# Optimization experiments

Hardware: AMD Instinct MI355X
Metric: run time of the kernel (lower is better)

Reference implementation:

```python
import jax, jax.numpy as jnp
import numpy as np


def setup_inputs() -> dict:
    key = jax.random.key(0)
    k1, k2, k3, k4 = jax.random.split(key, 4)
    B, T, C, H = 8, 2048, 1024, 128
    x = jax.random.normal(k1, (B, T, C), dtype=jnp.float32)
    Wq = jax.random.normal(k2, (C, H), dtype=jnp.float32) * (C ** -0.5)
    Wk = jax.random.normal(k3, (C, H), dtype=jnp.float32) * (C ** -0.5)
    Wv = jax.random.normal(k4, (C, H), dtype=jnp.float32) * (C ** -0.5)
    return {
        "x": x, "Wq": Wq, "Wk": Wk, "Wv": Wv,
        "gamma_fast_logit": jnp.float32(0.0),
        "gamma_medium_logit": jnp.float32(2.0),
        "gamma_slow_logit": jnp.float32(4.0),
        "alpha_logits": jnp.zeros((3,), dtype=jnp.float32),
    }


def _temporal_bias(T, gamma_fast_logit, gamma_medium_logit, gamma_slow_logit, alpha_logits):
    # delta_t[i,j] = max(i-j, 0)
    i = jnp.arange(T)[:, None]
    j = jnp.arange(T)[None, :]
    delta_t = jnp.maximum(i - j, 0).astype(jnp.float32)  # (T, T)
    gf = jax.nn.sigmoid(gamma_fast_logit) * 0.3 + 0.6
    gm = jax.nn.sigmoid(gamma_medium_logit) * 0.15 + 0.85
    gs = jax.nn.sigmoid(gamma_slow_logit) * 0.05 + 0.95
    alpha = jax.nn.softmax(alpha_logits)
    mix = (alpha[0] * jnp.power(gf, delta_t)
           + alpha[1] * jnp.power(gm, delta_t)
           + alpha[2] * jnp.power(gs, delta_t))
    return jnp.log(mix + 1e-8)  # (T, T)


def reference(x, Wq, Wk, Wv, gamma_fast_logit, gamma_medium_logit, gamma_slow_logit, alpha_logits):
    B, T, C = x.shape
    H = Wq.shape[1]
    q = x @ Wq  # (B, T, H)
    k = x @ Wk
    v = x @ Wv
    scale = H ** -0.5
    wei = jnp.einsum('bth,bsh->bts', q, k) * scale  # (B, T, T)
    bias = _temporal_bias(T, gamma_fast_logit, gamma_medium_logit, gamma_slow_logit, alpha_logits)
    wei = wei + bias[None, :, :]
    causal = jnp.tril(jnp.ones((T, T), dtype=bool))
    wei = jnp.where(causal[None, :, :], wei, -jnp.inf)
    wei = jax.nn.softmax(wei, axis=-1)
    out = jnp.einsum('bts,bsh->bth', wei, v)  # (B, T, H)
    return out
```

## Files before the change

### kernel.cpp

```cpp
#include <hip/hip_runtime.h>
#include <hip/hip_bf16.h>
#include <cstdint>

typedef __attribute__((ext_vector_type(8))) short bf16x8;
typedef __attribute__((ext_vector_type(4))) float f32x4;

#define T_SEQ 2048
#define NB    8
#define CDIM  1024
#define HDIM  128
#define NQB   32

__device__ __forceinline__ float exp2fast(float x) { return __builtin_amdgcn_exp2f(x); }
__device__ __forceinline__ float log2fast(float x) { return __builtin_amdgcn_logf(x); }

__device__ __forceinline__ short f2bf(float f) {
  unsigned u = __float_as_uint(f);
  u += 0x7fff + ((u >> 16) & 1);
  return (short)(u >> 16);
}

__device__ __forceinline__ unsigned pk2(float a, float b) {
  return (unsigned)(unsigned short)f2bf(a) | ((unsigned)(unsigned short)f2bf(b) << 16);
}

__device__ __forceinline__ void gload_lds16(const void* gsrc, void* lds_base_uniform) {
  __builtin_amdgcn_global_load_lds(
      (const __attribute__((address_space(1))) unsigned int*)gsrc,
      (__attribute__((address_space(3))) unsigned int*)lds_base_uniform,
      16, 0, 0);
}

__global__ void msta_bias_kernel(const float* gfl, const float* gml, const float* gsl,
                                 const float* al, float* tab) {
  int d = blockIdx.x * 256 + threadIdx.x;
  if (d >= T_SEQ) return;
  float gf = 0.30f / (1.f + __expf(-gfl[0])) + 0.60f;
  float gm = 0.15f / (1.f + __expf(-gml[0])) + 0.85f;
  float gs = 0.05f / (1.f + __expf(-gsl[0])) + 0.95f;
  float a0 = al[0], a1 = al[1], a2 = al[2];
  float mx = fmaxf(a0, fmaxf(a1, a2));
  float e0 = __expf(a0 - mx), e1 = __expf(a1 - mx), e2 = __expf(a2 - mx);
  float inv = 1.f / (e0 + e1 + e2);
  float fd = (float)d;
  float mix = e0 * inv * exp2fast(fd * log2fast(gf))
            + e1 * inv * exp2fast(fd * log2fast(gm))
            + e2 * inv * exp2fast(fd * log2fast(gs));
  tab[d] = log2fast(mix + 1e-8f);
}

__global__ void msta_wt_kernel(const float* Wq, const float* Wk, const float* Wv, short* wt) {
  int idx = blockIdx.x * 256 + threadIdx.x;
  int m = idx >> 17;
  int r = idx & 131071;
  int n = r >> 10;
  int kk = r & 1023;
  const float* W = (m == 0) ? Wq : ((m == 1) ? Wk : Wv);
  float v = W[kk * HDIM + n];
  if (m == 0) v *= 0.08838834764831845f * 1.4426950408889634f;
  wt[idx] = f2bf(v);
}

__global__ __launch_bounds__(256) void msta_qkv_kernel(
    const float* __restrict__ x, const short* __restrict__ wt,
    short* __restrict__ q, short* __restrict__ k, short* __restrict__ vt) {
  __shared__ short xs[2][64 * 64];
  __shared__ short wsm[2][128 * 64];

  const int tid  = threadIdx.x;
  const int lane = tid & 63;
  const int w    = tid >> 6;
  const int rh   = w >> 1, ch = w & 1;
  const int lo   = lane & 15, hi = lane >> 4;
  const int bid  = blockIdx.x;
  const int m    = bid % 3;
  const int r0   = (bid / 3) * 64;

  const int xG0 = tid * 2;
  const int xr0_ = xG0 >> 3, xg0_ = xG0 & 7;
  const int xr1_ = (xG0 + 1) >> 3, xg1_ = (xG0 + 1) & 7;
  const float* xsrc0 = x + (size_t)(r0 + xr0_) * CDIM + xg0_ * 8;
  const float* xsrc1 = x + (size_t)(r0 + xr1_) * CDIM + xg1_ * 8;
  const int xd0 = xr0_ * 128 + ((xg0_ ^ (xr0_ & 7)) << 4);
  const int xd1 = xr1_ * 128 + ((xg1_ ^ (xr1_ & 7)) << 4);

  const char* wsrc[4];
  #pragma unroll
  for (int i = 0; i < 4; i++) {
    int G = (w * 4 + i) * 64 + lane;
    int n = G >> 3, g = G & 7;
    int c = g ^ (n & 7);
    wsrc[i] = (const char*)(wt + ((size_t)m * 128 + n) * CDIM) + c * 16;
  }

  f32x4 acc[2][4];
  #pragma unroll
  for (int f = 0; f < 2; f++)
    #pragma unroll
    for (int jf = 0; jf < 4; jf++)
      acc[f][jf] = (f32x4){0.f, 0.f, 0.f, 0.f};

  float4 xa0, xb0, xa1, xb1;
  auto xload = [&](int t) {
    const float* s0 = xsrc0 + t * 64;
    const float* s1 = xsrc1 + t * 64;
    xa0 = *(const float4*)s0; xb0 = *(const float4*)(s0 + 4);
    xa1 = *(const float4*)s1; xb1 = *(const float4*)(s1 + 4);
  };
  auto xwrite = [&](int buf) {
    uint4 u0, u1;
    u0.x = pk2(xa0.x, xa0.y); u0.y = pk2(xa0.z, xa0.w);
    u0.z = pk2(xb0.x, xb0.y); u0.w = pk2(xb0.z, xb0.w);
    u1.x = pk2(xa1.x, xa1.y); u1.y = pk2(xa1.z, xa1.w);
    u1.z = pk2(xb1.x, xb1.y); u1.w = pk2(xb1.z, xb1.w);
    *(uint4*)((char*)xs[buf] + xd0) = u0;
    *(uint4*)((char*)xs[buf] + xd1) = u1;
  };
  auto stageW = [&](int buf) {
    char* wd = (char*)wsm[buf];
    #pragma unroll
    for (int i = 0; i < 4; i++) {
      gload_lds16(wsrc[i], wd + (w * 4 + i) * 1024);
      wsrc[i] += 128;
    }
  };

  xload(0);
  stageW(0);
  xwrite(0);
  __syncthreads();

  #pragma unroll 2
  for (int t = 0; t < 16; ++t) {
    const int buf = t & 1;
    if (t < 15) { xload(t + 1); stageW(buf ^ 1); }

    #pragma unroll
    for (int kk = 0; kk < 2; kk++) {
      bf16x8 A[2];
      #pragma unroll
      for (int f = 0; f < 2; f++) {
        int r = rh * 32 + f * 16 + lo;
        A[f] = *(const bf16x8*)((const char*)xs[buf] + r * 128 +
                                ((kk * 64 + hi * 16) ^ ((r & 7) << 4)));
      }
      #pragma unroll
      for (int jf = 0; jf < 4; jf++) {
        int n = ch * 64 + jf * 16 + lo;
        int byteoff = n * 128 + ((kk * 64 + hi * 16) ^ ((n & 7) << 4));
        bf16x8 Bv = *(const bf16x8*)((const char*)wsm[buf] + byteoff);
        acc[0][jf] = __builtin_amdgcn_mfma_f32_16x16x32_bf16(A[0], Bv, acc[0][jf], 0, 0, 0);
        acc[1][jf] = __builtin_amdgcn_mfma_f32_16x16x32_bf16(A[1], Bv, acc[1][jf], 0, 0, 0);
      }
    }
    if (t < 15) xwrite(buf ^ 1);
    __syncthreads();
  }

  #pragma unroll
  for (int f = 0; f < 2; f++) {
    #pragma unroll
    for (int jf = 0; jf < 4; jf++) {
      f32x4 a = acc[f][jf];
      int col = ch * 64 + jf * 16 + lo;
      int rbase = r0 + rh * 32 + f * 16 + hi * 4;
      if (m == 0) {
        #pragma unroll
        for (int rg = 0; rg < 4; rg++) q[(size_t)(rbase + rg) * HDIM + col] = f2bf(a[rg]);
      } else if (m == 1) {
        #pragma unroll
        for (int rg = 0; rg < 4; rg++) k[(size_t)(rbase + rg) * HDIM + col] = f2bf(a[rg]);
      } else {
        #pragma unroll
        for (int rg = 0; rg < 4; rg++) {
          int t = rbase + rg;
          vt[((size_t)(t >> 11) * HDIM + col) * T_SEQ + (t & 2047)] = f2bf(a[rg]);
        }
      }
    }
  }
}

template <int SP>
__global__ __launch_bounds__(256) void msta_attn_kernel(
    const short* __restrict__ q, const short* __restrict__ kg,
    const short* __restrict__ vt, const float* __restrict__ bias_tab,
    float* __restrict__ out, float* __restrict__ opart, float2* __restrict__ ml) {
  __shared__ short Ks[2][64 * 128];
  __shared__ short Vs[2][128 * 64];
  __shared__ short Ps[4][16 * 64];

  const int tid  = threadIdx.x;
  const int lane = tid & 63;
  const int w    = tid >> 6;
  const int lo   = lane & 15, hi = lane >> 4;

  const int idx = blockIdx.x;
  const int qb  = (NQB - 1) - idx / (NB * SP);
  const int rem = idx % (NB * SP);
  const int b   = rem / SP;
  const int sp  = rem % SP;
  const int q0  = qb * 64;

  const int nt  = qb + 1;
  const int csz = (nt + SP - 1) / SP;
  const int t0  = sp * csz;
  const int t1  = (t0 + csz < nt) ? (t0 + csz) : nt;

  if (t0 >= t1) {
    if (SP > 1 && lane < 16) {
      int t = q0 + w * 16 + lane;
      ml[((size_t)sp * NB + b) * T_SEQ + t] = make_float2(-1e30f, 0.f);
    }
    return;
  }

  const short* kb = kg + (size_t)b * T_SEQ * HDIM;
  const short* vb = vt + (size_t)b * HDIM * T_SEQ;

  bf16x8 qf[4];
  const short* qbase = q + ((size_t)b * T_SEQ + q0 + w * 16 + lo) * HDIM;
  #pragma unroll
  for (int ks = 0; ks < 4; ks++)
    qf[ks] = *(const bf16x8*)(qbase + ks * 32 + hi * 8);

  const int s0i = (t1 - 1) * 64;
  const char* ksrc[4];
  const char* vsrc[4];
  #pragma unroll
  for (int i = 0; i < 4; i++) {
    int G = (w * 4 + i) * 64 + lane;
    { int r = G >> 4, g = G & 15;
      int c = (g & 8) | ((g & 7) ^ (r & 7));
      ksrc[i] = (const char*)(kb + (size_t)(s0i + r) * HDIM) + c * 16; }
    { int r = G >> 3, g = G & 7;
      int c = g ^ (r & 7);
      vsrc[i] = (const char*)(vb + (size_t)r * T_SEQ + s0i) + c * 16; }
  }
  auto stage = [&](int buf) {
    char* kd = (char*)Ks[buf];
    char* vd = (char*)Vs[buf];
    #pragma unroll
    for (int i = 0; i < 4; i++) {
      gload_lds16(ksrc[i], kd + (w * 4 + i) * 1024);
      ksrc[i] -= 64 * HDIM * 2;
      gload_lds16(vsrc[i], vd + (w * 4 + i) * 1024);
      vsrc[i] -= 128;
    }
  };

  f32x4 oacc[8];
  #pragma unroll
  for (int jo = 0; jo < 8; jo++) oacc[jo] = (f32x4){0.f, 0.f, 0.f, 0.f};
  float mrow[4], lrow[4];
  #pragma unroll
  for (int rg = 0; rg < 4; rg++) { mrow[rg] = -1e30f; lrow[rg] = 0.f; }

  stage(0);
  __syncthreads();

  int cur = 0;
  for (int t = t1 - 1; t >= t0; --t, cur ^= 1) {
    if (t > t0) stage(cur ^ 1);
    const int s0 = t * 64;

    f32x4 sacc[4];
    #pragma unroll
    for (int jf = 0; jf < 4; jf++) sacc[jf] = (f32x4){0.f, 0.f, 0.f, 0.f};
    __builtin_amdgcn_s_setprio(1);
    #pragma unroll
    for (int ks = 0; ks < 4; ks++) {
      #pragma unroll
      for (int jf = 0; jf < 4; jf++) {
        int s = jf * 16 + lo;
        int byteoff = s * 256 + ((ks * 64 + hi * 16) ^ ((s & 7) << 4));
        bf16x8 kf = *(const bf16x8*)((const char*)Ks[cur] + byteoff);
        sacc[jf] = __builtin_amdgcn_mfma_f32_16x16x32_bf16(qf[ks], kf, sacc[jf], 0, 0, 0);
      }
    }
    __builtin_amdgcn_s_setprio(0);

    float sv[4][4];
    #pragma unroll
    for (int jf = 0; jf < 4; jf++) {
      #pragma unroll
      for (int rg = 0; rg < 4; rg++) {
        int i_ = q0 + w * 16 + hi * 4 + rg;
        int j_ = s0 + jf * 16 + lo;
        int d = i_ - j_;
        sv[jf][rg] = (d >= 0) ? (sacc[jf][rg] + bias_tab[d]) : -1e30f;
      }
    }

    float mx[4];
    bool need = false;
    #pragma unroll
    for (int rg = 0; rg < 4; rg++) {
      float v = fmaxf(fmaxf(sv[0][rg], sv[1][rg]), fmaxf(sv[2][rg], sv[3][rg]));
      v = fmaxf(v, __shfl_xor(v, 1));
      v = fmaxf(v, __shfl_xor(v, 2));
      v = fmaxf(v, __shfl_xor(v, 4));
      v = fmaxf(v, __shfl_xor(v, 8));
      mx[rg] = v;
      need |= (v > mrow[rg]);
    }
    if (__any((int)need)) {
      #pragma unroll
      for (int rg = 0; rg < 4; rg++) {
        float mnew = fmaxf(mrow[rg], mx[rg]);
        float sc = exp2fast(mrow[rg] - mnew);
        mrow[rg] = mnew;
        lrow[rg] *= sc;
        #pragma unroll
        for (int jo = 0; jo < 8; jo++) oacc[jo][rg] *= sc;
      }
    }

    float psum[4] = {0.f, 0.f, 0.f, 0.f};
    #pragma unroll
    for (int jf = 0; jf < 4; jf++) {
      #pragma unroll
      for (int rg = 0; rg < 4; rg++) {
        float p = exp2fast(sv[jf][rg] - mrow[rg]);
        psum[rg] += p;
        int prow = hi * 4 + rg;
        int pcol = jf * 16 + lo;
        int byteoff = prow * 128 + ((pcol * 2) ^ ((prow & 7) << 4));
        *(short*)((char*)Ps[w] + byteoff) = f2bf(p);
      }
    }
    #pragma unroll
    for (int rg = 0; rg < 4; rg++) {
      float s = psum[rg];
      s += __shfl_xor(s, 1); s += __shfl_xor(s, 2);
      s += __shfl_xor(s, 4); s += __shfl_xor(s, 8);
      lrow[rg] += s;
    }

    __builtin_amdgcn_s_setprio(1);
    #pragma unroll
    for (int ks = 0; ks < 2; ks++) {
      int pbyte = lo * 128 + ((ks * 64 + hi * 16) ^ ((lo & 7) << 4));
      bf16x8 pf = *(const bf16x8*)((const char*)Ps[w] + pbyte);
      #pragma unroll
      for (int jo = 0; jo < 8; jo++) {
        int h = jo * 16 + lo;
        int vbyte = h * 128 + ((ks * 64 + hi * 16) ^ ((h & 7) << 4));
        bf16x8 vf = *(const bf16x8*)((const char*)Vs[cur] + vbyte);
        oacc[jo] = __builtin_amdgcn_mfma_f32_16x16x32_bf16(pf, vf, oacc[jo], 0, 0, 0);
      }
    }
    __builtin_amdgcn_s_setprio(0);
    __syncthreads();
  }

  if constexpr (SP == 1) {
    #pragma unroll
    for (int jo = 0; jo < 8; jo++) {
      #pragma unroll
      for (int rg = 0; rg < 4; rg++) {
        int t = q0 + w * 16 + hi * 4 + rg;
        out[((size_t)b * T_SEQ + t) * HDIM + jo * 16 + lo] = oacc[jo][rg] / lrow[rg];
      }
    }
  } else {
    #pragma unroll
    for (int jo = 0; jo < 8; jo++) {
      #pragma unroll
      for (int rg = 0; rg < 4; rg++) {
        int t = q0 + w * 16 + hi * 4 + rg;
        opart[(((size_t)sp * NB + b) * T_SEQ + t) * HDIM + jo * 16 + lo] = oacc[jo][rg];
      }
    }
    if (lo == 0) {
      #pragma unroll
      for (int rg = 0; rg < 4; rg++) {
        int t = q0 + w * 16 + hi * 4 + rg;
        ml[((size_t)sp * NB + b) * T_SEQ + t] = make_float2(mrow[rg], lrow[rg]);
      }
    }
  }
}

template <int SP>
__global__ __launch_bounds__(256) void msta_merge_kernel(
    const float* __restrict__ opart, const float2* __restrict__ ml,
    float* __restrict__ out) {
  int id  = blockIdx.x * 256 + threadIdx.x;
  int row = id >> 5;
  int c4  = id & 31;

  float2 v[SP];
  float m = -1e30f;
  #pragma unroll
  for (int sp = 0; sp < SP; sp++) {
    v[sp] = ml[(size_t)sp * (NB * T_SEQ) + row];
    if (v[sp].y > 0.f) m = fmaxf(m, v[sp].x);
  }
  float denom = 0.f;
  float wgt[SP];
  #pragma unroll
  for (int sp = 0; sp < SP; sp++) {
    wgt[sp] = (v[sp].y > 0.f) ? exp2fast(v[sp].x - m) : 0.f;
    denom += wgt[sp] * v[sp].y;
  }
  float4 acc = {0.f, 0.f, 0.f, 0.f};
  #pragma unroll
  for (int sp = 0; sp < SP; sp++) {
    if (wgt[sp] != 0.f) {
      float4 o = *(const float4*)(opart + ((size_t)sp * (NB * T_SEQ) + row) * HDIM + c4 * 4);
      acc.x += wgt[sp] * o.x; acc.y += wgt[sp] * o.y;
      acc.z += wgt[sp] * o.z; acc.w += wgt[sp] * o.w;
    }
  }
  float inv = 1.f / denom;
  float4 r = make_float4(acc.x * inv, acc.y * inv, acc.z * inv, acc.w * inv);
  *(float4*)(out + (size_t)row * HDIM + c4 * 4) = r;
}

extern "C" void kernel_launch(void* const* d_in, const int* in_sizes, int n_in,
                              void* d_out, int out_size, void* d_ws, size_t ws_size,
                              hipStream_t stream) {
  (void)in_sizes; (void)n_in; (void)out_size;
  const float* x   = (const float*)d_in[0];
  const float* Wq  = (const float*)d_in[1];
  const float* Wk  = (const float*)d_in[2];
  const float* Wv  = (const float*)d_in[3];
  const float* gfl = (const float*)d_in[4];
  const float* gml = (const float*)d_in[5];
  const float* gsl = (const float*)d_in[6];
  const float* al  = (const float*)d_in[7];
  float* out = (float*)d_out;

  char* wsb = (char*)d_ws;
  float*  bias_tab = (float*)wsb;
  short*  qw   = (short*)(wsb + 8192);
  short*  kw   = (short*)(wsb + 8192 + 1 * 4194304);
  short*  vtw  = (short*)(wsb + 8192 + 2 * 4194304);
  short*  wtw  = (short*)(wsb + 8192 + 3 * 4194304);
  float*  opart = (float*)(wsb + 13639680);
  float2* mlp   = (float2*)(wsb + 47194112);
  const size_t need4 = 47194112 + 524288;

  msta_bias_kernel<<<8, 256, 0, stream>>>(gfl, gml, gsl, al, bias_tab);
  msta_wt_kernel<<<1536, 256, 0, stream>>>(Wq, Wk, Wv, wtw);
  msta_qkv_kernel<<<768, 256, 0, stream>>>(x, wtw, qw, kw, vtw);

  if (ws_size >= need4) {
    msta_attn_kernel<4><<<NB * NQB * 4, 256, 0, stream>>>(qw, kw, vtw, bias_tab,
                                                          nullptr, opart, mlp);
    msta_merge_kernel<4><<<(NB * T_SEQ * 32) / 256, 256, 0, stream>>>(opart, mlp, out);
  } else {
    msta_attn_kernel<1><<<NB * NQB, 256, 0, stream>>>(qw, kw, vtw, bias_tab,
                                                      out, nullptr, nullptr);
  }
}
```

Measured before the change: 99.73 us.

## Load MFMA operands directly from global memory, dropping LDS staging

```diff
diff --git a/kernel.cpp b/kernel.cpp
--- a/kernel.cpp
+++ b/kernel.cpp
@@ -64,7 +64,6 @@
 __global__ __launch_bounds__(256) void msta_qkv_kernel(
     const float* __restrict__ x, const short* __restrict__ wt,
     short* __restrict__ q, short* __restrict__ k, short* __restrict__ vt) {
-  __shared__ short xs[2][64 * 64];
   __shared__ short wsm[2][128 * 64];
 
   const int tid  = threadIdx.x;
@@ -72,17 +71,14 @@
   const int w    = tid >> 6;
   const int rh   = w >> 1, ch = w & 1;
   const int lo   = lane & 15, hi = lane >> 4;
+
   const int bid  = blockIdx.x;
-  const int m    = bid % 3;
-  const int r0   = (bid / 3) * 64;
-
-  const int xG0 = tid * 2;
-  const int xr0_ = xG0 >> 3, xg0_ = xG0 & 7;
-  const int xr1_ = (xG0 + 1) >> 3, xg1_ = (xG0 + 1) & 7;
-  const float* xsrc0 = x + (size_t)(r0 + xr0_) * CDIM + xg0_ * 8;
-  const float* xsrc1 = x + (size_t)(r0 + xr1_) * CDIM + xg1_ * 8;
-  const int xd0 = xr0_ * 128 + ((xg0_ ^ (xr0_ & 7)) << 4);
-  const int xd1 = xr1_ * 128 + ((xg1_ ^ (xr1_ & 7)) << 4);
+  const int xcd  = bid & 7;
+  const int j    = bid >> 3;
+  const int m    = j % 3;
+  const int r0   = (xcd * 32 + j / 3) * 64;
+
+  const float* xbase = x + (size_t)(r0 + rh * 32 + lo) * CDIM + hi * 8;
 
   const char* wsrc[4];
   #pragma unroll
@@ -100,21 +96,16 @@
     for (int jf = 0; jf < 4; jf++)
       acc[f][jf] = (f32x4){0.f, 0.f, 0.f, 0.f};
 
-  float4 xa0, xb0, xa1, xb1;
-  auto xload = [&](int t) {
-    const float* s0 = xsrc0 + t * 64;
-    const float* s1 = xsrc1 + t * 64;
-    xa0 = *(const float4*)s0; xb0 = *(const float4*)(s0 + 4);
-    xa1 = *(const float4*)s1; xb1 = *(const float4*)(s1 + 4);
-  };
-  auto xwrite = [&](int buf) {
-    uint4 u0, u1;
-    u0.x = pk2(xa0.x, xa0.y); u0.y = pk2(xa0.z, xa0.w);
-    u0.z = pk2(xb0.x, xb0.y); u0.w = pk2(xb0.z, xb0.w);
-    u1.x = pk2(xa1.x, xa1.y); u1.y = pk2(xa1.z, xa1.w);
-    u1.z = pk2(xb1.x, xb1.y); u1.w = pk2(xb1.z, xb1.w);
-    *(uint4*)((char*)xs[buf] + xd0) = u0;
-    *(uint4*)((char*)xs[buf] + xd1) = u1;
+  float4 F0[2][2][2], F1[2][2][2];
+  auto xfetch = [&](int t, float4 (&F)[2][2][2]) {
+    #pragma unroll
+    for (int f = 0; f < 2; f++)
+      #pragma unroll
+      for (int kk = 0; kk < 2; kk++) {
+        const float* p = xbase + (size_t)f * 16 * CDIM + t * 64 + kk * 32;
+        F[f][kk][0] = *(const float4*)p;
+        F[f][kk][1] = *(const float4*)(p + 4);
+      }
   };
   auto stageW = [&](int buf) {
     char* wd = (char*)wsm[buf];
@@ -124,36 +115,41 @@
       wsrc[i] += 128;
     }
   };
-
-  xload(0);
-  stageW(0);
-  xwrite(0);
-  __syncthreads();
-
-  #pragma unroll 2
-  for (int t = 0; t < 16; ++t) {
-    const int buf = t & 1;
-    if (t < 15) { xload(t + 1); stageW(buf ^ 1); }
-
+  auto compute = [&](const float4 (&F)[2][2][2], int wbuf) {
     #pragma unroll
     for (int kk = 0; kk < 2; kk++) {
       bf16x8 A[2];
       #pragma unroll
       for (int f = 0; f < 2; f++) {
-        int r = rh * 32 + f * 16 + lo;
-        A[f] = *(const bf16x8*)((const char*)xs[buf] + r * 128 +
-                                ((kk * 64 + hi * 16) ^ ((r & 7) << 4)));
+        uint4 u;
+        u.x = pk2(F[f][kk][0].x, F[f][kk][0].y);
+        u.y = pk2(F[f][kk][0].z, F[f][kk][0].w);
+        u.z = pk2(F[f][kk][1].x, F[f][kk][1].y);
+        u.w = pk2(F[f][kk][1].z, F[f][kk][1].w);
+        A[f] = *(bf16x8*)&u;
       }
       #pragma unroll
       for (int jf = 0; jf < 4; jf++) {
         int n = ch * 64 + jf * 16 + lo;
         int byteoff = n * 128 + ((kk * 64 + hi * 16) ^ ((n & 7) << 4));
-        bf16x8 Bv = *(const bf16x8*)((const char*)wsm[buf] + byteoff);
+        bf16x8 Bv = *(const bf16x8*)((const char*)wsm[wbuf] + byteoff);
         acc[0][jf] = __builtin_amdgcn_mfma_f32_16x16x32_bf16(A[0], Bv, acc[0][jf], 0, 0, 0);
         acc[1][jf] = __builtin_amdgcn_mfma_f32_16x16x32_bf16(A[1], Bv, acc[1][jf], 0, 0, 0);
       }
     }
-    if (t < 15) xwrite(buf ^ 1);
+  };
+
+  xfetch(0, F0);
+  stageW(0);
+  __syncthreads();
+
+  for (int t = 0; t < 16; t += 2) {
+    xfetch(t + 1, F1);
+    stageW(1);
+    compute(F0, 0);
+    __syncthreads();
+    if (t + 2 < 16) { xfetch(t + 2, F0); stageW(0); }
+    compute(F1, 1);
     __syncthreads();
   }
 
@@ -173,8 +169,8 @@
       } else {
         #pragma unroll
         for (int rg = 0; rg < 4; rg++) {
-          int t = rbase + rg;
-          vt[((size_t)(t >> 11) * HDIM + col) * T_SEQ + (t & 2047)] = f2bf(a[rg]);
+          int t2 = rbase + rg;
+          vt[((size_t)(t2 >> 11) * HDIM + col) * T_SEQ + (t2 & 2047)] = f2bf(a[rg]);
         }
       }
     }
@@ -186,8 +182,6 @@
     const short* __restrict__ q, const short* __restrict__ kg,
     const short* __restrict__ vt, const float* __restrict__ bias_tab,
     float* __restrict__ out, float* __restrict__ opart, float2* __restrict__ ml) {
-  __shared__ short Ks[2][64 * 128];
-  __shared__ short Vs[2][128 * 64];
   __shared__ short Ps[4][16 * 64];
 
   const int tid  = threadIdx.x;
@@ -224,30 +218,8 @@
   for (int ks = 0; ks < 4; ks++)
     qf[ks] = *(const bf16x8*)(qbase + ks * 32 + hi * 8);
 
-  const int s0i = (t1 - 1) * 64;
-  const char* ksrc[4];
-  const char* vsrc[4];
-  #pragma unroll
-  for (int i = 0; i < 4; i++) {
-    int G = (w * 4 + i) * 64 + lane;
-    { int r = G >> 4, g = G & 15;
-      int c = (g & 8) | ((g & 7) ^ (r & 7));
-      ksrc[i] = (const char*)(kb + (size_t)(s0i + r) * HDIM) + c * 16; }
-    { int r = G >> 3, g = G & 7;
-      int c = g ^ (r & 7);
-      vsrc[i] = (const char*)(vb + (size_t)r * T_SEQ + s0i) + c * 16; }
-  }
-  auto stage = [&](int buf) {
-    char* kd = (char*)Ks[buf];
-    char* vd = (char*)Vs[buf];
-    #pragma unroll
-    for (int i = 0; i < 4; i++) {
-      gload_lds16(ksrc[i], kd + (w * 4 + i) * 1024);
-      ksrc[i] -= 64 * HDIM * 2;
-      gload_lds16(vsrc[i], vd + (w * 4 + i) * 1024);
-      vsrc[i] -= 128;
-    }
-  };
+  const short* kfb = kb + (size_t)lo * HDIM + hi * 8;
+  const short* vfb = vb + (size_t)lo * T_SEQ + hi * 8;
 
   f32x4 oacc[8];
   #pragma unroll
@@ -256,12 +228,7 @@
   #pragma unroll
   for (int rg = 0; rg < 4; rg++) { mrow[rg] = -1e30f; lrow[rg] = 0.f; }
 
-  stage(0);
-  __syncthreads();
-
-  int cur = 0;
-  for (int t = t1 - 1; t >= t0; --t, cur ^= 1) {
-    if (t > t0) stage(cur ^ 1);
+  for (int t = t1 - 1; t >= t0; --t) {
     const int s0 = t * 64;
 
     f32x4 sacc[4];
@@ -272,9 +239,7 @@
     for (int ks = 0; ks < 4; ks++) {
       #pragma unroll
       for (int jf = 0; jf < 4; jf++) {
-        int s = jf * 16 + lo;
-        int byteoff = s * 256 + ((ks * 64 + hi * 16) ^ ((s & 7) << 4));
-        bf16x8 kf = *(const bf16x8*)((const char*)Ks[cur] + byteoff);
+        bf16x8 kf = *(const bf16x8*)(kfb + (size_t)(s0 + jf * 16) * HDIM + ks * 32);
         sacc[jf] = __builtin_amdgcn_mfma_f32_16x16x32_bf16(qf[ks], kf, sacc[jf], 0, 0, 0);
       }
     }
@@ -344,14 +309,11 @@
       bf16x8 pf = *(const bf16x8*)((const char*)Ps[w] + pbyte);
       #pragma unroll
       for (int jo = 0; jo < 8; jo++) {
-        int h = jo * 16 + lo;
-        int vbyte = h * 128 + ((ks * 64 + hi * 16) ^ ((h & 7) << 4));
-        bf16x8 vf = *(const bf16x8*)((const char*)Vs[cur] + vbyte);
+        bf16x8 vf = *(const bf16x8*)(vfb + (size_t)(jo * 16) * T_SEQ + s0 + ks * 32);
         oacc[jo] = __builtin_amdgcn_mfma_f32_16x16x32_bf16(pf, vf, oacc[jo], 0, 0, 0);
       }
     }
     __builtin_amdgcn_s_setprio(0);
-    __syncthreads();
   }
 
   if constexpr (SP == 1) {
```

Measured after the change: 166.6 us. +67.1%, slower.

## Raise KV split to 8, store partials in bf16, single-buffer LDS, XCD-aware QKV mapping

Applied to the files above, without the earlier changes.

```diff
diff --git a/kernel.cpp b/kernel.cpp
--- a/kernel.cpp
+++ b/kernel.cpp
@@ -18,6 +18,10 @@
   unsigned u = __float_as_uint(f);
   u += 0x7fff + ((u >> 16) & 1);
   return (short)(u >> 16);
+}
+
+__device__ __forceinline__ float bf2f(short s) {
+  return __uint_as_float(((unsigned)(unsigned short)s) << 16);
 }
 
 __device__ __forceinline__ unsigned pk2(float a, float b) {
@@ -73,8 +77,10 @@
   const int rh   = w >> 1, ch = w & 1;
   const int lo   = lane & 15, hi = lane >> 4;
   const int bid  = blockIdx.x;
-  const int m    = bid % 3;
-  const int r0   = (bid / 3) * 64;
+  const int xcd  = bid & 7;
+  const int j    = bid >> 3;
+  const int m    = j % 3;
+  const int r0   = (xcd * 32 + j / 3) * 64;
 
   const int xG0 = tid * 2;
   const int xr0_ = xG0 >> 3, xg0_ = xG0 & 7;
@@ -185,9 +191,9 @@
 __global__ __launch_bounds__(256) void msta_attn_kernel(
     const short* __restrict__ q, const short* __restrict__ kg,
     const short* __restrict__ vt, const float* __restrict__ bias_tab,
-    float* __restrict__ out, float* __restrict__ opart, float2* __restrict__ ml) {
-  __shared__ short Ks[2][64 * 128];
-  __shared__ short Vs[2][128 * 64];
+    float* __restrict__ out, short* __restrict__ opart, float2* __restrict__ ml) {
+  __shared__ short Ks[64 * 128];
+  __shared__ short Vs[128 * 64];
   __shared__ short Ps[4][16 * 64];
 
   const int tid  = threadIdx.x;
@@ -237,14 +243,12 @@
       int c = g ^ (r & 7);
       vsrc[i] = (const char*)(vb + (size_t)r * T_SEQ + s0i) + c * 16; }
   }
-  auto stage = [&](int buf) {
-    char* kd = (char*)Ks[buf];
-    char* vd = (char*)Vs[buf];
+  auto stage = [&]() {
     #pragma unroll
     for (int i = 0; i < 4; i++) {
-      gload_lds16(ksrc[i], kd + (w * 4 + i) * 1024);
+      gload_lds16(ksrc[i], (char*)Ks + (w * 4 + i) * 1024);
       ksrc[i] -= 64 * HDIM * 2;
-      gload_lds16(vsrc[i], vd + (w * 4 + i) * 1024);
+      gload_lds16(vsrc[i], (char*)Vs + (w * 4 + i) * 1024);
       vsrc[i] -= 128;
     }
   };
@@ -256,12 +260,10 @@
   #pragma unroll
   for (int rg = 0; rg < 4; rg++) { mrow[rg] = -1e30f; lrow[rg] = 0.f; }
 
-  stage(0);
+  stage();
   __syncthreads();
 
-  int cur = 0;
-  for (int t = t1 - 1; t >= t0; --t, cur ^= 1) {
-    if (t > t0) stage(cur ^ 1);
+  for (int t = t1 - 1; t >= t0; --t) {
     const int s0 = t * 64;
 
     f32x4 sacc[4];
@@ -274,7 +276,7 @@
       for (int jf = 0; jf < 4; jf++) {
         int s = jf * 16 + lo;
         int byteoff = s * 256 + ((ks * 64 + hi * 16) ^ ((s & 7) << 4));
-        bf16x8 kf = *(const bf16x8*)((const char*)Ks[cur] + byteoff);
+        bf16x8 kf = *(const bf16x8*)((const char*)Ks + byteoff);
         sacc[jf] = __builtin_amdgcn_mfma_f32_16x16x32_bf16(qf[ks], kf, sacc[jf], 0, 0, 0);
       }
     }
@@ -346,12 +348,17 @@
       for (int jo = 0; jo < 8; jo++) {
         int h = jo * 16 + lo;
         int vbyte = h * 128 + ((ks * 64 + hi * 16) ^ ((h & 7) << 4));
-        bf16x8 vf = *(const bf16x8*)((const char*)Vs[cur] + vbyte);
+        bf16x8 vf = *(const bf16x8*)((const char*)Vs + vbyte);
         oacc[jo] = __builtin_amdgcn_mfma_f32_16x16x32_bf16(pf, vf, oacc[jo], 0, 0, 0);
       }
     }
     __builtin_amdgcn_s_setprio(0);
-    __syncthreads();
+
+    if (t > t0) {
+      __syncthreads();
+      stage();
+      __syncthreads();
+    }
   }
 
   if constexpr (SP == 1) {
@@ -369,7 +376,7 @@
       #pragma unroll
       for (int rg = 0; rg < 4; rg++) {
         int t = q0 + w * 16 + hi * 4 + rg;
-        opart[(((size_t)sp * NB + b) * T_SEQ + t) * HDIM + jo * 16 + lo] = oacc[jo][rg];
+        opart[(((size_t)sp * NB + b) * T_SEQ + t) * HDIM + jo * 16 + lo] = f2bf(oacc[jo][rg]);
       }
     }
     if (lo == 0) {
@@ -384,7 +391,7 @@
 
 template <int SP>
 __global__ __launch_bounds__(256) void msta_merge_kernel(
-    const float* __restrict__ opart, const float2* __restrict__ ml,
+    const short* __restrict__ opart, const float2* __restrict__ ml,
     float* __restrict__ out) {
   int id  = blockIdx.x * 256 + threadIdx.x;
   int row = id >> 5;
@@ -408,9 +415,9 @@
   #pragma unroll
   for (int sp = 0; sp < SP; sp++) {
     if (wgt[sp] != 0.f) {
-      float4 o = *(const float4*)(opart + ((size_t)sp * (NB * T_SEQ) + row) * HDIM + c4 * 4);
-      acc.x += wgt[sp] * o.x; acc.y += wgt[sp] * o.y;
-      acc.z += wgt[sp] * o.z; acc.w += wgt[sp] * o.w;
+      ushort4 o = *(const ushort4*)(opart + ((size_t)sp * (NB * T_SEQ) + row) * HDIM + c4 * 4);
+      acc.x += wgt[sp] * bf2f((short)o.x); acc.y += wgt[sp] * bf2f((short)o.y);
+      acc.z += wgt[sp] * bf2f((short)o.z); acc.w += wgt[sp] * bf2f((short)o.w);
     }
   }
   float inv = 1.f / denom;
@@ -438,15 +445,22 @@
   short*  kw   = (short*)(wsb + 8192 + 1 * 4194304);
   short*  vtw  = (short*)(wsb + 8192 + 2 * 4194304);
   short*  wtw  = (short*)(wsb + 8192 + 3 * 4194304);
-  float*  opart = (float*)(wsb + 13639680);
-  float2* mlp   = (float2*)(wsb + 47194112);
-  const size_t need4 = 47194112 + 524288;
+  short*  opart = (short*)(wsb + 13639680);
+
+  const size_t need8 = 13639680 + 8ull * 4194304 + 8ull * 131072;
+  const size_t need4 = 13639680 + 4ull * 4194304 + 4ull * 131072;
 
   msta_bias_kernel<<<8, 256, 0, stream>>>(gfl, gml, gsl, al, bias_tab);
   msta_wt_kernel<<<1536, 256, 0, stream>>>(Wq, Wk, Wv, wtw);
   msta_qkv_kernel<<<768, 256, 0, stream>>>(x, wtw, qw, kw, vtw);
 
-  if (ws_size >= need4) {
+  if (ws_size >= need8) {
+    float2* mlp = (float2*)(wsb + 13639680 + 8ull * 4194304);
+    msta_attn_kernel<8><<<NB * NQB * 8, 256, 0, stream>>>(qw, kw, vtw, bias_tab,
+                                                          nullptr, opart, mlp);
+    msta_merge_kernel<8><<<(NB * T_SEQ * 32) / 256, 256, 0, stream>>>(opart, mlp, out);
+  } else if (ws_size >= need4) {
+    float2* mlp = (float2*)(wsb + 13639680 + 4ull * 4194304);
     msta_attn_kernel<4><<<NB * NQB * 4, 256, 0, stream>>>(qw, kw, vtw, bias_tab,
                                                           nullptr, opart, mlp);
     msta_merge_kernel<4><<<(NB * T_SEQ * 32) / 256, 256, 0, stream>>>(opart, mlp, out);
```

New measurement: 88.78 us. 1.12x faster.
